# Performance work log

Measured on AMD Instinct MI355X. Metric: run time of the kernel, lower is better.

The kernel has to match this reference:

```python
import jax, jax.numpy as jnp
import numpy as np

H = 2048
E = 8
K = 2
INTER = 2048
T = 2048


def setup_inputs() -> dict:
    key = jax.random.key(0)
    k1, k2, k3 = jax.random.split(key, 3)
    hidden_4d = jax.random.normal(k1, (1, 1, T, H), dtype=jnp.float32)
    # learned per-expert fused gate+up projection: [1, E, H, 2*inter]
    gate_up_proj = jax.random.normal(k2, (1, E, H, INTER * 2), dtype=jnp.float32) * 0.02
    # binary (expert, token) dispatch mask: on average K of E experts active per token
    sparsity = (jax.random.uniform(k3, (1, E, T, 1)) < (K / E)).astype(jnp.float32)
    return {"hidden_4d": hidden_4d, "gate_up_proj": gate_up_proj, "sparsity": sparsity}


def reference(hidden_4d, gate_up_proj, sparsity):
    # sparse_matmul semantics: per-expert GEMM of tokens against expert weight
    # blocks, with output blocks zeroed (skipped) where the sparsity mask is 0.
    # hidden_4d: [1, 1, T, H]; gate_up_proj: [1, E, H, F]; sparsity: [1, E, T, 1]
    # out[a, e, t, f] = mask[a, e, t] * sum_h hidden[a, 0, t, h] * W[a, e, h, f]
    out = jnp.einsum("abth,aehf->aetf", hidden_4d, gate_up_proj) * sparsity
    return out.sum()
```

## Files before the change

### kernel.cpp

```cpp
#include <hip/hip_runtime.h>

#define H_DIM 2048
#define E_DIM 8
#define T_DIM 2048
#define F_DIM 4096
#define NBLK  1024
#define HCHUNK 16

typedef float f32x4 __attribute__((ext_vector_type(4)));

__global__ __launch_bounds__(256, 4) void moe_dot(
    const float* __restrict__ hidden,
    const float* __restrict__ W,
    const float* __restrict__ mask,
    float* __restrict__ out) {
  const int tid  = threadIdx.x;
  const int bid  = blockIdx.x;
  const int e    = bid >> 7;
  const int h0   = (bid & 127) * HCHUNK;
  const int wave = tid >> 6;
  const int lane = tid & 63;

  __shared__ float m_lds[T_DIM];
  __shared__ float A_val[HCHUNK];
  __shared__ float wsum[4];

  const size_t wbase = ((size_t)e * H_DIM + h0) * F_DIM;
  const int awave = bid & 3;

  if (wave == awave) {
    const f32x4* m4 = (const f32x4*)(mask + (size_t)e * T_DIM);
    f32x4* l4 = (f32x4*)m_lds;
    #pragma unroll
    for (int i = 0; i < 8; ++i) l4[lane + (i << 6)] = m4[lane + (i << 6)];

    const int hq  = lane & 3;
    const int ttg = lane >> 2;
    const float* hp = hidden + h0 + (hq << 2);
    f32x4 accA = (f32x4)0.f;
    #pragma unroll 8
    for (int k = 0; k < 128; ++k) {
      int t = ttg + (k << 4);
      accA += *(const f32x4*)(hp + (size_t)t * H_DIM) * m_lds[t];
    }
    #pragma unroll
    for (int off = 4; off <= 32; off <<= 1) {
      accA.x += __shfl_down(accA.x, off, 64);
      accA.y += __shfl_down(accA.y, off, 64);
      accA.z += __shfl_down(accA.z, off, 64);
      accA.w += __shfl_down(accA.w, off, 64);
    }
    if (lane < 4) ((f32x4*)A_val)[lane] = accA;
  }

  const int r0 = wave << 2;
  const f32x4* rp = (const f32x4*)(W + wbase + (size_t)r0 * F_DIM);
  f32x4 a0 = (f32x4)0.f, a1 = (f32x4)0.f, a2 = (f32x4)0.f, a3 = (f32x4)0.f;
  #pragma unroll 4
  for (int i = 0; i < 16; ++i) {
    int idx = lane + (i << 6);
    a0 += rp[idx];
    a1 += rp[idx + 1024];
    a2 += rp[idx + 2048];
    a3 += rp[idx + 3072];
  }
  float s0 = (a0.x + a0.y) + (a0.z + a0.w);
  float s1 = (a1.x + a1.y) + (a1.z + a1.w);
  float s2 = (a2.x + a2.y) + (a2.z + a2.w);
  float s3 = (a3.x + a3.y) + (a3.z + a3.w);
  #pragma unroll
  for (int off = 32; off > 0; off >>= 1) {
    s0 += __shfl_down(s0, off, 64);
    s1 += __shfl_down(s1, off, 64);
    s2 += __shfl_down(s2, off, 64);
    s3 += __shfl_down(s3, off, 64);
  }

  __syncthreads();
  if (lane == 0)
    wsum[wave] = s0 * A_val[r0]     + s1 * A_val[r0 + 1]
               + s2 * A_val[r0 + 2] + s3 * A_val[r0 + 3];
  __syncthreads();
  if (tid == 0)
    atomicAdd(out, (wsum[0] + wsum[1]) + (wsum[2] + wsum[3]));
}

extern "C" void kernel_launch(void* const* d_in, const int* in_sizes, int n_in,
                              void* d_out, int out_size, void* d_ws, size_t ws_size,
                              hipStream_t stream) {
  const float* hidden = (const float*)d_in[0];
  const float* W      = (const float*)d_in[1];
  const float* mask   = (const float*)d_in[2];
  float* out = (float*)d_out;

  hipMemsetAsync(d_out, 0, sizeof(float), stream);
  moe_dot<<<NBLK, 256, 0, stream>>>(hidden, W, mask, out);
}
```

Before: 378.9 us.

## Split masked hidden reduction across all four waves and stagger W streaming

Each wave now computes the masked token-sum of hidden for its own four h rows, reading the mask directly from global memory, instead of one wave doing all 16 rows via an LDS-staged mask. This removes the LDS mask copy, the single-wave serial bottleneck and one block barrier. The W row-sum loop is split so each wave streams a wave-dependent number of iterations before its hidden reduction, staggering memory traffic across waves. Hidden and mask reads become strided per-lane loads of four floats each, which may coalesce less well.

New measurement: 419.5 us. 1.11x slower.

```diff
diff --git a/kernel.cpp b/kernel.cpp
--- a/kernel.cpp
+++ b/kernel.cpp
@@ -21,49 +21,41 @@
   const int wave = tid >> 6;
   const int lane = tid & 63;
 
-  __shared__ float m_lds[T_DIM];
-  __shared__ float A_val[HCHUNK];
   __shared__ float wsum[4];
 
-  const size_t wbase = ((size_t)e * H_DIM + h0) * F_DIM;
-  const int awave = bid & 3;
+  const int r0 = wave << 2;
+  const f32x4* rp = (const f32x4*)(W + ((size_t)e * H_DIM + h0 + r0) * F_DIM);
+  const float* hp = hidden + h0 + r0;
+  const float* mp = mask + (size_t)e * T_DIM + lane;
 
-  if (wave == awave) {
-    const f32x4* m4 = (const f32x4*)(mask + (size_t)e * T_DIM);
-    f32x4* l4 = (f32x4*)m_lds;
-    #pragma unroll
-    for (int i = 0; i < 8; ++i) l4[lane + (i << 6)] = m4[lane + (i << 6)];
+  f32x4 a0 = (f32x4)0.f, a1 = (f32x4)0.f, a2 = (f32x4)0.f, a3 = (f32x4)0.f;
+  f32x4 accA = (f32x4)0.f;
 
-    const int hq  = lane & 3;
-    const int ttg = lane >> 2;
-    const float* hp = hidden + h0 + (hq << 2);
-    f32x4 accA = (f32x4)0.f;
-    #pragma unroll 8
-    for (int k = 0; k < 128; ++k) {
-      int t = ttg + (k << 4);
-      accA += *(const f32x4*)(hp + (size_t)t * H_DIM) * m_lds[t];
-    }
-    #pragma unroll
-    for (int off = 4; off <= 32; off <<= 1) {
-      accA.x += __shfl_down(accA.x, off, 64);
-      accA.y += __shfl_down(accA.y, off, 64);
-      accA.z += __shfl_down(accA.z, off, 64);
-      accA.w += __shfl_down(accA.w, off, 64);
-    }
-    if (lane < 4) ((f32x4*)A_val)[lane] = accA;
-  }
-
-  const int r0 = wave << 2;
-  const f32x4* rp = (const f32x4*)(W + wbase + (size_t)r0 * F_DIM);
-  f32x4 a0 = (f32x4)0.f, a1 = (f32x4)0.f, a2 = (f32x4)0.f, a3 = (f32x4)0.f;
-  #pragma unroll 4
-  for (int i = 0; i < 16; ++i) {
+  int i = 0;
+  #pragma unroll 1
+  for (; i < wave; ++i) {
     int idx = lane + (i << 6);
     a0 += rp[idx];
     a1 += rp[idx + 1024];
     a2 += rp[idx + 2048];
     a3 += rp[idx + 3072];
   }
+
+  #pragma unroll 4
+  for (int k = 0; k < 32; ++k) {
+    int t = lane + (k << 6);
+    accA += *(const f32x4*)(hp + (size_t)t * H_DIM) * mp[(size_t)(k << 6)];
+  }
+
+  #pragma unroll 2
+  for (; i < 16; ++i) {
+    int idx = lane + (i << 6);
+    a0 += rp[idx];
+    a1 += rp[idx + 1024];
+    a2 += rp[idx + 2048];
+    a3 += rp[idx + 3072];
+  }
+
   float s0 = (a0.x + a0.y) + (a0.z + a0.w);
   float s1 = (a1.x + a1.y) + (a1.z + a1.w);
   float s2 = (a2.x + a2.y) + (a2.z + a2.w);
@@ -74,12 +66,13 @@
     s1 += __shfl_down(s1, off, 64);
     s2 += __shfl_down(s2, off, 64);
     s3 += __shfl_down(s3, off, 64);
+    accA.x += __shfl_down(accA.x, off, 64);
+    accA.y += __shfl_down(accA.y, off, 64);
+    accA.z += __shfl_down(accA.z, off, 64);
+    accA.w += __shfl_down(accA.w, off, 64);
   }
-
-  __syncthreads();
   if (lane == 0)
-    wsum[wave] = s0 * A_val[r0]     + s1 * A_val[r0 + 1]
-               + s2 * A_val[r0 + 2] + s3 * A_val[r0 + 3];
+    wsum[wave] = s0 * accA.x + s1 * accA.y + s2 * accA.z + s3 * accA.w;
   __syncthreads();
   if (tid == 0)
     atomicAdd(out, (wsum[0] + wsum[1]) + (wsum[2] + wsum[3]));
```
